# Kernel optimization log

Hardware: AMD Instinct MI355X
Metric: run time of the kernel (lower is better)

## Reference

```python
import jax, jax.numpy as jnp
import numpy as np

B, S, D, HD = 16, 2048, 1024, 64  # batch, seq, n_embd, head_dim


def setup_inputs() -> dict:
    key = jax.random.key(0)
    ks = jax.random.split(key, 4)
    std = 1.0 / np.sqrt(D)
    return {
        "x": jax.random.normal(ks[0], (B, S, D), dtype=jnp.float32),
        "Wq": jax.random.normal(ks[1], (D, HD), dtype=jnp.float32) * std,
        "bq": jnp.zeros((HD,), dtype=jnp.float32),
        "Wk": jax.random.normal(ks[2], (D, HD), dtype=jnp.float32) * std,
        "bk": jnp.zeros((HD,), dtype=jnp.float32),
        "Wv": jax.random.normal(ks[3], (D, HD), dtype=jnp.float32) * std,
        "bv": jnp.zeros((HD,), dtype=jnp.float32),
    }


def reference(x, Wq, bq, Wk, bk, Wv, bv):
    q = x @ Wq + bq  # [B,S,HD]
    k = x @ Wk + bk
    v = x @ Wv + bv
    scale = jnp.asarray(HD, x.dtype) ** -0.5
    scores = jnp.einsum("bqd,bkd->bqk", q, k) * scale  # [B,S,S]
    seq = x.shape[1]
    causal = jnp.tril(jnp.ones((seq, seq), dtype=bool))  # True = keep
    scores = jnp.where(causal, scores, jnp.asarray(-jnp.inf, scores.dtype))
    probs = jax.nn.softmax(scores, axis=-1)
    return jnp.einsum("bqk,bkd->bqd", probs, v)  # [B,S,HD]
```

## Files before the change

kernel.cpp:

```cpp
#include <hip/hip_runtime.h>
#include <hip/hip_bf16.h>
#include <math.h>

constexpr int Bsz  = 16;
constexpr int Seq  = 2048;
constexpr int Din  = 1024;
constexpr int Hd   = 64;
constexpr int Rows = Bsz * Seq;

typedef short  short8 __attribute__((ext_vector_type(8)));
typedef float  f32x4  __attribute__((ext_vector_type(4)));

__device__ __forceinline__ short bf16_bits(float f) {
    __hip_bfloat16 h = __float2bfloat16(f);
    return __builtin_bit_cast(short, h);
}

typedef __attribute__((address_space(1))) const void gvoid_t;
typedef __attribute__((address_space(3))) void lvoid_t;
__device__ __forceinline__ void gll16(const void* g, void* l) {
    __builtin_amdgcn_global_load_lds((gvoid_t*)g, (lvoid_t*)l, 16, 0, 0);
}

__global__ __launch_bounds__(256) void wt_prep(
    const float* __restrict__ Wq, const float* __restrict__ Wk,
    const float* __restrict__ Wv, short* __restrict__ Wf)
{
    const int u     = blockIdx.x * 256 + threadIdx.x;
    const int chunk = u / 768;
    const int rem   = u - chunk * 768;
    const int f     = rem >> 6;
    const int lane  = rem & 63;
    const int wg    = f >> 2, nt = f & 3;
    const int quad  = lane >> 4, l16 = lane & 15;
    const float* W  = (wg == 0) ? Wq : (wg == 1) ? Wk : Wv;
    const int k0 = chunk * 32 + quad * 8;
    const int n  = nt * 16 + l16;
    short8 v;
    #pragma unroll
    for (int j = 0; j < 8; ++j) v[j] = bf16_bits(W[(size_t)(k0 + j) * Hd + n]);
    *(short8*)(Wf + (size_t)u * 8) = v;
}

__global__ __launch_bounds__(256) void qkv_kernel(
    const float* __restrict__ x,
    const short* __restrict__ Wf,
    const float* __restrict__ bq, const float* __restrict__ bk,
    const float* __restrict__ bv,
    short* __restrict__ Qf, short* __restrict__ Kf, short* __restrict__ Vf)
{
    const int tid  = threadIdx.x;
    const int wave = tid >> 6;
    const int lane = tid & 63;
    const int quad = lane >> 4;
    const int l16  = lane & 15;
    const int g    = wave >> 1;
    const int h    = wave & 1;
    const int bx   = blockIdx.x;
    const int m0   = bx * 32;

    __shared__ __align__(16) short smem[12288];
    short* sW = smem;

    const float* xrow = x + (size_t)(m0 + g * 16 + l16) * Din + quad * 8;

    f32x4 acc[6] = {};

    {
        const short* gp = Wf + wave * 1536 + lane * 8;
        short*       lp = sW + wave * 1536;
        gll16(gp,        lp);
        gll16(gp +  512, lp +  512);
        gll16(gp + 1024, lp + 1024);
    }
    float4 a0 = *(const float4*)(xrow);
    float4 a1 = *(const float4*)(xrow + 4);
    __syncthreads();

    for (int c = 0; c < 32; ++c) {
        const int cur = (c & 1) * 6144;
        if (c < 31) {
            const short* gp = Wf + (size_t)(c + 1) * 6144 + wave * 1536 + lane * 8;
            short*       lp = sW + (cur ^ 6144) + wave * 1536;
            gll16(gp,        lp);
            gll16(gp +  512, lp +  512);
            gll16(gp + 1024, lp + 1024);
        }
        float4 b0 = a0, b1 = a1;
        if (c < 31) {
            b0 = *(const float4*)(xrow + (c + 1) * 32);
            b1 = *(const float4*)(xrow + (c + 1) * 32 + 4);
        }
        short8 af;
        af[0] = bf16_bits(a0.x); af[1] = bf16_bits(a0.y);
        af[2] = bf16_bits(a0.z); af[3] = bf16_bits(a0.w);
        af[4] = bf16_bits(a1.x); af[5] = bf16_bits(a1.y);
        af[6] = bf16_bits(a1.z); af[7] = bf16_bits(a1.w);
        const short* wsrc = sW + cur + h * 3072 + lane * 8;
        #pragma unroll
        for (int i = 0; i < 6; ++i) {
            const short8 bb = *(const short8*)(wsrc + i * 512);
            acc[i] = __builtin_amdgcn_mfma_f32_16x16x32_bf16(af, bb, acc[i], 0, 0, 0);
        }
        a0 = b0; a1 = b1;
        __syncthreads();
    }

    short (*eS)[2][1152] = reinterpret_cast<short(*)[2][1152]>(smem);
    short* eV = smem + 4608;

    if (h == 0) {
        #pragma unroll
        for (int nt = 0; nt < 4; ++nt) {
            const float bb = bq[nt * 16 + l16];
            #pragma unroll
            for (int r = 0; r < 4; ++r)
                eS[g][0][(quad * 4 + r) * 72 + nt * 16 + l16] =
                    bf16_bits(acc[nt][r] + bb);
        }
        #pragma unroll
        for (int nt = 0; nt < 2; ++nt) {
            const float bb = bk[nt * 16 + l16];
            #pragma unroll
            for (int r = 0; r < 4; ++r)
                eS[g][1][(quad * 4 + r) * 72 + nt * 16 + l16] =
                    bf16_bits(acc[4 + nt][r] + bb);
        }
        const short8 v0 = *(const short8*)&eS[g][0][l16 * 72 + quad * 8];
        const short8 v1 = *(const short8*)&eS[g][0][l16 * 72 + 32 + quad * 8];
        const size_t tg = (size_t)bx * 2 + g;
        *(short8*)(Qf + (tg * 2 + 0) * 512 + lane * 8) = v0;
        *(short8*)(Qf + (tg * 2 + 1) * 512 + lane * 8) = v1;
    } else {
        #pragma unroll
        for (int nt = 0; nt < 2; ++nt) {
            const float bb = bk[(2 + nt) * 16 + l16];
            #pragma unroll
            for (int r = 0; r < 4; ++r)
                eS[g][1][(quad * 4 + r) * 72 + (2 + nt) * 16 + l16] =
                    bf16_bits(acc[nt][r] + bb);
        }
        #pragma unroll
        for (int nt = 0; nt < 4; ++nt) {
            const float bb = bv[nt * 16 + l16];
            #pragma unroll
            for (int r = 0; r < 4; ++r)
                eV[(nt * 16 + l16) * 44 + g * 16 + quad * 4 + r] =
                    bf16_bits(acc[2 + nt][r] + bb);
        }
    }
    __syncthreads();

    if (h == 0) {
        const short8 v0 = *(const short8*)&eS[g][1][l16 * 72 + quad * 8];
        const short8 v1 = *(const short8*)&eS[g][1][l16 * 72 + 32 + quad * 8];
        const size_t t  = bx >> 1;
        const int    nt = (bx & 1) * 2 + g;
        *(short8*)(Kf + ((t * 2 + 0) * 4 + nt) * 512 + lane * 8) = v0;
        *(short8*)(Kf + ((t * 2 + 1) * 4 + nt) * 512 + lane * 8) = v1;
    }
    {
        const size_t t  = bx >> 1;
        const int    ks = bx & 1;
        const short8 v  = *(const short8*)&eV[(wave * 16 + l16) * 44 + quad * 8];
        *(short8*)(Vf + ((t * 2 + ks) * 4 + wave) * 512 + lane * 8) = v;
    }
}

__global__ __launch_bounds__(256) void attn_kernel(
    const short* __restrict__ Qf, const short* __restrict__ Kf,
    const short* __restrict__ Vf, float* __restrict__ out)
{
    const int tid  = threadIdx.x;
    const int wave = tid >> 6;
    const int lane = tid & 63;
    const int quad = lane >> 4;
    const int l16  = lane & 15;
    const int b    = blockIdx.y;
    const int bx   = blockIdx.x;
    const int qs   = (bx & 1) ? (127 - (bx >> 1)) : (bx >> 1);
    const int dTile = qs >> 2;
    const int tiles = dTile + 1;
    const int qoff  = (qs & 3) * 16;

    __shared__ __align__(16) unsigned char sm[17408 + 512];
    short* Ps   = (short*)sm;
    float* Obuf = (float*)sm;
    float* mb   = (float*)(sm + 17408);
    float* lb   = mb + 64;

    const size_t tg = (size_t)b * 128 + qs;
    const short8 qf0 = *(const short8*)(Qf + (tg * 2 + 0) * 512 + lane * 8);
    const short8 qf1 = *(const short8*)(Qf + (tg * 2 + 1) * 512 + lane * 8);

    f32x4 o[4] = {};
    float m_run[4], l_run[4];
    #pragma unroll
    for (int r = 0; r < 4; ++r) { m_run[r] = -INFINITY; l_run[r] = 0.0f; }

    const float C = 0.125f * 1.44269504088896340736f;

    for (int kt = wave; kt < tiles; kt += 4) {
        const short* ktile = Kf + (size_t)(b * 32 + kt) * 4096;
        const short* vtile = Vf + (size_t)(b * 32 + kt) * 4096;

        f32x4 s[4] = {};
        __builtin_amdgcn_s_setprio(1);
        #pragma unroll
        for (int nt = 0; nt < 4; ++nt) {
            const short8 kf0 = *(const short8*)(ktile + ((0 * 4 + nt) * 64 + lane) * 8);
            const short8 kf1 = *(const short8*)(ktile + ((1 * 4 + nt) * 64 + lane) * 8);
            s[nt] = __builtin_amdgcn_mfma_f32_16x16x32_bf16(qf0, kf0, s[nt], 0, 0, 0);
            s[nt] = __builtin_amdgcn_mfma_f32_16x16x32_bf16(qf1, kf1, s[nt], 0, 0, 0);
        }
        __builtin_amdgcn_s_setprio(0);

        if (kt == dTile) {
            #pragma unroll
            for (int nt = 0; nt < 4; ++nt) {
                const int kg = nt * 16 + l16;
                #pragma unroll
                for (int r = 0; r < 4; ++r) {
                    const int qg = qoff + quad * 4 + r;
                    s[nt][r] = (kg <= qg) ? s[nt][r] * C : -INFINITY;
                }
            }
        } else {
            #pragma unroll
            for (int nt = 0; nt < 4; ++nt)
                #pragma unroll
                for (int r = 0; r < 4; ++r) s[nt][r] *= C;
        }

        float rm[4];
        #pragma unroll
        for (int r = 0; r < 4; ++r)
            rm[r] = fmaxf(fmaxf(s[0][r], s[1][r]), fmaxf(s[2][r], s[3][r]));
        #pragma unroll
        for (int off = 1; off < 16; off <<= 1)
            #pragma unroll
            for (int r = 0; r < 4; ++r)
                rm[r] = fmaxf(rm[r], __shfl_xor(rm[r], off));

        float alpha[4];
        #pragma unroll
        for (int r = 0; r < 4; ++r) {
            const float mn = fmaxf(m_run[r], rm[r]);
            alpha[r] = exp2f(m_run[r] - mn);
            m_run[r] = mn;
        }

        float rs[4] = {0.f, 0.f, 0.f, 0.f};
        #pragma unroll
        for (int nt = 0; nt < 4; ++nt)
            #pragma unroll
            for (int r = 0; r < 4; ++r) {
                const float p = exp2f(s[nt][r] - m_run[r]);
                s[nt][r] = p;
                rs[r] += p;
            }
        #pragma unroll
        for (int off = 1; off < 16; off <<= 1)
            #pragma unroll
            for (int r = 0; r < 4; ++r)
                rs[r] += __shfl_xor(rs[r], off);
        #pragma unroll
        for (int r = 0; r < 4; ++r) l_run[r] = l_run[r] * alpha[r] + rs[r];

        #pragma unroll
        for (int r = 0; r < 4; ++r) {
            o[0][r] *= alpha[r]; o[1][r] *= alpha[r];
            o[2][r] *= alpha[r]; o[3][r] *= alpha[r];
        }

        #pragma unroll
        for (int nt = 0; nt < 4; ++nt)
            #pragma unroll
            for (int r = 0; r < 4; ++r)
                Ps[wave * 1152 + (quad * 4 + r) * 72 + nt * 16 + l16] = bf16_bits(s[nt][r]);

        const short8 pf0 = *(const short8*)&Ps[wave * 1152 + l16 * 72 + quad * 8];
        const short8 pf1 = *(const short8*)&Ps[wave * 1152 + l16 * 72 + 32 + quad * 8];

        __builtin_amdgcn_s_setprio(1);
        #pragma unroll
        for (int nt = 0; nt < 4; ++nt) {
            const short8 vA = *(const short8*)(vtile + ((0 * 4 + nt) * 64 + lane) * 8);
            const short8 vB = *(const short8*)(vtile + ((1 * 4 + nt) * 64 + lane) * 8);
            o[nt] = __builtin_amdgcn_mfma_f32_16x16x32_bf16(pf0, vA, o[nt], 0, 0, 0);
            o[nt] = __builtin_amdgcn_mfma_f32_16x16x32_bf16(pf1, vB, o[nt], 0, 0, 0);
        }
        __builtin_amdgcn_s_setprio(0);
    }

    if (l16 == 0) {
        #pragma unroll
        for (int r = 0; r < 4; ++r) mb[wave * 16 + quad * 4 + r] = m_run[r];
    }
    __syncthreads();

    float fac[4];
    #pragma unroll
    for (int r = 0; r < 4; ++r) {
        const int row = quad * 4 + r;
        const float mg = fmaxf(fmaxf(mb[row], mb[16 + row]),
                               fmaxf(mb[32 + row], mb[48 + row]));
        fac[r] = exp2f(m_run[r] - mg);
    }
    if (l16 == 0) {
        #pragma unroll
        for (int r = 0; r < 4; ++r) lb[wave * 16 + quad * 4 + r] = l_run[r] * fac[r];
    }
    #pragma unroll
    for (int nt = 0; nt < 4; ++nt)
        #pragma unroll
        for (int r = 0; r < 4; ++r)
            Obuf[wave * 1088 + (quad * 4 + r) * 68 + nt * 16 + l16] = o[nt][r] * fac[r];
    __syncthreads();

    {
        const int row = tid >> 4;
        const int c0  = (tid & 15) * 4;
        const float lsum = lb[row] + lb[16 + row] + lb[32 + row] + lb[48 + row];
        float4 a = *(const float4*)&Obuf[0 * 1088 + row * 68 + c0];
        const float4 a1 = *(const float4*)&Obuf[1 * 1088 + row * 68 + c0];
        const float4 a2 = *(const float4*)&Obuf[2 * 1088 + row * 68 + c0];
        const float4 a3 = *(const float4*)&Obuf[3 * 1088 + row * 68 + c0];
        a.x += a1.x + a2.x + a3.x;  a.y += a1.y + a2.y + a3.y;
        a.z += a1.z + a2.z + a3.z;  a.w += a1.w + a2.w + a3.w;
        const float inv = 1.0f / lsum;
        float4 r4 = make_float4(a.x * inv, a.y * inv, a.z * inv, a.w * inv);
        *(float4*)(out + ((size_t)b * Seq + qs * 16 + row) * Hd + c0) = r4;
    }
}

extern "C" void kernel_launch(void* const* d_in, const int* in_sizes, int n_in,
                              void* d_out, int out_size, void* d_ws, size_t ws_size,
                              hipStream_t stream)
{
    const float* x  = (const float*)d_in[0];
    const float* Wq = (const float*)d_in[1];
    const float* bq = (const float*)d_in[2];
    const float* Wk = (const float*)d_in[3];
    const float* bk = (const float*)d_in[4];
    const float* Wv = (const float*)d_in[5];
    const float* bv = (const float*)d_in[6];
    float* out = (float*)d_out;

    short* Qf = (short*)d_ws;
    short* Kf = Qf + (size_t)Rows * Hd;
    short* Vf = Kf + (size_t)Rows * Hd;
    short* Wf = Vf + (size_t)Rows * Hd;

    wt_prep<<<96, 256, 0, stream>>>(Wq, Wk, Wv, Wf);
    qkv_kernel<<<1024, 256, 0, stream>>>(x, Wf, bq, bk, bv, Qf, Kf, Vf);
    attn_kernel<<<dim3(128, 16), 256, 0, stream>>>(Qf, Kf, Vf, out);
}
```

Baseline: 288.9 us.

## Triple-buffer weight LDS loads in QKV projection with partial vmcnt waits

The QKV projection loop moves from double to triple buffering of the weight tiles in shared memory and prefetches x rows two iterations ahead. Full __syncthreads are replaced with s_waitcnt vmcnt(N) plus s_barrier, so each iteration waits only for the oldest outstanding loads. This hides more global-load latency at the cost of 50% more LDS per block and relies on hand-counted vmcnt values being correct.

```diff
diff --git a/kernel.cpp b/kernel.cpp
--- a/kernel.cpp
+++ b/kernel.cpp
@@ -59,7 +59,7 @@
     const int bx   = blockIdx.x;
     const int m0   = bx * 32;
 
-    __shared__ __align__(16) short smem[12288];
+    __shared__ __align__(16) short smem[18432];
     short* sW = smem;
 
     const float* xrow = x + (size_t)(m0 + g * 16 + l16) * Din + quad * 8;
@@ -72,38 +72,57 @@
         gll16(gp,        lp);
         gll16(gp +  512, lp +  512);
         gll16(gp + 1024, lp + 1024);
-    }
+        const short* gp1 = gp + 6144;
+        short*       lp1 = lp + 6144;
+        gll16(gp1,        lp1);
+        gll16(gp1 +  512, lp1 +  512);
+        gll16(gp1 + 1024, lp1 + 1024);
+    }
+    asm volatile("" ::: "memory");
     float4 a0 = *(const float4*)(xrow);
     float4 a1 = *(const float4*)(xrow + 4);
-    __syncthreads();
-
+    float4 b0 = *(const float4*)(xrow + 32);
+    float4 b1 = *(const float4*)(xrow + 36);
+    asm volatile("s_waitcnt vmcnt(7)" ::: "memory");
+    __builtin_amdgcn_s_barrier();
+
+    int rd = 0;
+    int st = 2;
     for (int c = 0; c < 32; ++c) {
-        const int cur = (c & 1) * 6144;
-        if (c < 31) {
-            const short* gp = Wf + (size_t)(c + 1) * 6144 + wave * 1536 + lane * 8;
-            short*       lp = sW + (cur ^ 6144) + wave * 1536;
+        if (c + 2 < 32) {
+            const short* gp = Wf + (size_t)(c + 2) * 6144 + wave * 1536 + lane * 8;
+            short*       lp = sW + st * 6144 + wave * 1536;
             gll16(gp,        lp);
             gll16(gp +  512, lp +  512);
             gll16(gp + 1024, lp + 1024);
         }
-        float4 b0 = a0, b1 = a1;
-        if (c < 31) {
-            b0 = *(const float4*)(xrow + (c + 1) * 32);
-            b1 = *(const float4*)(xrow + (c + 1) * 32 + 4);
+        asm volatile("" ::: "memory");
+        float4 n0 = b0, n1 = b1;
+        if (c + 2 < 32) {
+            n0 = *(const float4*)(xrow + (c + 2) * 32);
+            n1 = *(const float4*)(xrow + (c + 2) * 32 + 4);
         }
         short8 af;
         af[0] = bf16_bits(a0.x); af[1] = bf16_bits(a0.y);
         af[2] = bf16_bits(a0.z); af[3] = bf16_bits(a0.w);
         af[4] = bf16_bits(a1.x); af[5] = bf16_bits(a1.y);
         af[6] = bf16_bits(a1.z); af[7] = bf16_bits(a1.w);
-        const short* wsrc = sW + cur + h * 3072 + lane * 8;
+        const short* wsrc = sW + rd * 6144 + h * 3072 + lane * 8;
         #pragma unroll
         for (int i = 0; i < 6; ++i) {
             const short8 bb = *(const short8*)(wsrc + i * 512);
             acc[i] = __builtin_amdgcn_mfma_f32_16x16x32_bf16(af, bb, acc[i], 0, 0, 0);
         }
-        a0 = b0; a1 = b1;
-        __syncthreads();
+        a0 = b0; a1 = b1; b0 = n0; b1 = n1;
+        rd = (rd == 2) ? 0 : rd + 1;
+        st = (st == 2) ? 0 : st + 1;
+        if (c < 30) {
+            asm volatile("s_waitcnt vmcnt(7) lgkmcnt(0)" ::: "memory");
+            __builtin_amdgcn_s_barrier();
+        } else if (c == 30) {
+            asm volatile("s_waitcnt vmcnt(2) lgkmcnt(0)" ::: "memory");
+            __builtin_amdgcn_s_barrier();
+        }
     }
 
     short (*eS)[2][1152] = reinterpret_cast<short(*)[2][1152]>(smem);
```

New measurement: 282.5 us. 1.02x faster.
